# Performance work log

Hardware: AMD Instinct MI355X
Metric: run time of the kernel (lower is better)

The kernel has to match this reference:

```python
import jax, jax.numpy as jnp
import numpy as np


def _bd(x, W, b):
    # block-diagonal linear: x [B, D] -> [B, Dout], W [H, D/H, Dout/H], b [Dout]
    B, D = x.shape
    H = W.shape[0]
    y = jnp.einsum('bhi,hio->bho', x.reshape(B, H, D // H), W)
    return y.reshape(B, -1) + b


def setup_inputs() -> dict:
    key = jax.random.key(0)
    ks = jax.random.split(key, 16)
    B, D, H = 8192, 1024, 8
    U = int(D * 4 / 3)  # 1365
    d = D // H          # 128
    s = 0.05
    f32 = jnp.float32
    return {
        'x': jax.random.normal(ks[0], (B, D), f32),
        'h_prev': jax.random.normal(ks[1], (B, D), f32),
        'c_prev': jax.random.normal(ks[2], (B, D), f32),
        'n_prev': jax.random.uniform(ks[3], (B, D), f32) + 0.5,  # positive normalizer state
        'm_prev': jax.random.normal(ks[4], (B, D), f32),
        'ln_g': jnp.ones((D,), f32),
        'ln_b': jnp.zeros((D,), f32),
        'conv_w': jax.random.normal(ks[5], (1, 1, 4), f32) * 0.5,
        'conv_b': jax.random.normal(ks[6], (1,), f32) * 0.1,
        'W': jax.random.normal(ks[7], (4, H, d, d), f32) * s,   # gates z,i,f,o input projections
        'bW': jax.random.normal(ks[8], (4, D), f32) * s,
        'R': jax.random.normal(ks[9], (4, H, d, d), f32) * s,   # gates z,i,f,o recurrent projections
        'bR': jax.random.normal(ks[10], (4, D), f32) * s,
        'upl_w': jax.random.normal(ks[11], (D, U), f32) * s,
        'upl_b': jnp.zeros((U,), f32),
        'upr_w': jax.random.normal(ks[12], (D, U), f32) * s,
        'upr_b': jnp.zeros((U,), f32),
        'down_w': jax.random.normal(ks[13], (U, D), f32) * s,
        'down_b': jnp.zeros((D,), f32),
    }


def reference(x, h_prev, c_prev, n_prev, m_prev, ln_g, ln_b, conv_w, conv_b,
              W, bW, R, bR, upl_w, upl_b, upr_w, upr_b, down_w, down_b):
    # LayerNorm over feature dim (eps matches torch default 1e-5)
    mu = jnp.mean(x, axis=-1, keepdims=True)
    var = jnp.var(x, axis=-1, keepdims=True)
    x_norm = (x - mu) * jax.lax.rsqrt(var + 1e-5) * ln_g + ln_b
    # causal conv1d along the feature axis: kernel 4, left-pad 3 (Conv1d(1,1,4))
    conv = jax.lax.conv_general_dilated(
        x_norm[:, None, :], conv_w, window_strides=(1,), padding=[(3, 0)],
        dimension_numbers=('NCH', 'OIH', 'NCH'))[:, 0, :] + conv_b
    x_conv = jax.nn.silu(conv)
    # block-diagonal gate pre-activations (gate order in W/R stacks: z, i, f, o)
    z = jnp.tanh(_bd(x, W[0], bW[0]) + _bd(h_prev, R[0], bR[0]))
    o = jax.nn.sigmoid(_bd(x, W[3], bW[3]) + _bd(h_prev, R[3], bR[3]))
    i_tilde = _bd(x_conv, W[1], bW[1]) + _bd(h_prev, R[1], bR[1])
    f_tilde = _bd(x_conv, W[2], bW[2]) + _bd(h_prev, R[2], bR[2])
    # stabilized exp-max gating
    m_t = jnp.maximum(f_tilde + m_prev, i_tilde)
    i = jnp.exp(i_tilde - m_t)
    f = jnp.exp(f_tilde + m_prev - m_t)
    c_t = f * c_prev + i * z
    n_t = f * n_prev + i
    h_t = o * c_t / n_t
    # gated MLP (torch F.gelu default = exact erf gelu)
    left = h_t @ upl_w + upl_b
    right = jax.nn.gelu(h_t @ upr_w + upr_b, approximate=False)
    output = (left * right) @ down_w + down_b
    return (output, h_t, c_t, n_t, m_t)
```

## Files before the change

### kernel.cpp

```cpp
#include <hip/hip_runtime.h>
#include <hip/hip_bf16.h>

typedef __attribute__((ext_vector_type(8))) short s8v;
typedef __attribute__((ext_vector_type(4))) float f4v;
typedef unsigned short us4 __attribute__((ext_vector_type(4)));

#define NB 8192
#define ND 1024
#define NH 8
#define NU 1365
#define NUP 1408
#define GK 384
#define GN 512
static const size_t BD = (size_t)NB * ND;

#define WS_AG   ((size_t)0)
#define WS_G    ((size_t)50331648)
#define WS_HBF  ((size_t)73400320)
#define WS_WG   ((size_t)90177536)
#define WS_ULR  ((size_t)93323264)
#define WS_DWNT ((size_t)99090432)

__device__ __forceinline__ void gload16(const void* g, void* l) {
  __builtin_amdgcn_global_load_lds((const __attribute__((address_space(1))) void*)g,
                                   (__attribute__((address_space(3))) void*)l, 16, 0, 0);
}
__device__ __forceinline__ unsigned short tobf(float f) {
  unsigned int u = __float_as_uint(f);
  unsigned int r = (u + 0x7FFFu + ((u >> 16) & 1u)) >> 16;
  return (unsigned short)r;
}
__device__ __forceinline__ float frcp(float x) { return __builtin_amdgcn_rcpf(x); }
__device__ __forceinline__ float fsigm(float x) { return frcp(1.f + __expf(-x)); }
__device__ __forceinline__ float ftanh(float x) {
  float e = __expf(2.f * x);
  return 1.f - 2.f * frcp(e + 1.f);
}
__device__ __forceinline__ f4v mfma16(s8v a, s8v b, f4v c) {
  return __builtin_amdgcn_mfma_f32_16x16x32_bf16(a, b, c, 0, 0, 0);
}

__global__ __launch_bounds__(256) void prep_norm(
    const float* __restrict__ W, const float* __restrict__ R,
    const float* __restrict__ upl, const float* __restrict__ upr,
    const float* __restrict__ dwn,
    const float* __restrict__ x, const float* __restrict__ hp,
    const float* __restrict__ lg, const float* __restrict__ lb,
    const float* __restrict__ cw, const float* __restrict__ cb,
    unsigned short* __restrict__ Wg, unsigned short* __restrict__ ULR,
    unsigned short* __restrict__ Dt, unsigned short* __restrict__ Ag) {
  if (blockIdx.x < 23040) {
    long long idx = (long long)blockIdx.x * 256 + threadIdx.x;
    const long long N1 = (long long)4096 * GK;
    const long long N3 = (long long)2 * NUP * ND;
    const long long N2 = (long long)NUP * ND;
    if (idx < N1) {
      int c = (int)(idx / GK), k = (int)(idx % GK);
      int j = c & 15, g = (c >> 4) & 3, cgrp = (c >> 6) & 7, h = c >> 9;
      int o = cgrp * 16 + j;
      float v = 0.f;
      if (k < 128) {
        if (g == 0 || g == 3) v = W[(((size_t)g * NH + h) * 128 + k) * 128 + o];
      } else if (k < 256) {
        if (g == 1 || g == 2) v = W[(((size_t)g * NH + h) * 128 + (k - 128)) * 128 + o];
      } else {
        v = R[(((size_t)g * NH + h) * 128 + (k - 256)) * 128 + o];
      }
      Wg[idx] = tobf(v);
      return;
    }
    idx -= N1;
    if (idx < N3) {
      int r = (int)(idx / ND), k = (int)(idx % ND);
      int o = (r >> 4) & 1;
      int gcol = (r >> 5) * 16 + (r & 15);
      float v = 0.f;
      if (gcol < NU) v = o ? upr[(size_t)k * NU + gcol] : upl[(size_t)k * NU + gcol];
      ULR[idx] = tobf(v);
      return;
    }
    idx -= N3;
    if (idx < N2) { int n = (int)(idx / NUP), k = (int)(idx % NUP);
      Dt[idx] = (k < NU) ? tobf(dwn[(size_t)k * ND + n]) : 0; }
    return;
  }
  const int b = blockIdx.x - 23040, tid = threadIdx.x;
  const int lane = tid & 63, wv = tid >> 6;
  __shared__ float xs[1024];
  __shared__ float red[8];
  const int d0 = tid * 4;
  float4 xv = *(const float4*)(x + (size_t)b * ND + d0);
  float s = xv.x + xv.y + xv.z + xv.w;
  float ss = xv.x * xv.x + xv.y * xv.y + xv.z * xv.z + xv.w * xv.w;
#pragma unroll
  for (int o = 32; o; o >>= 1) { s += __shfl_down(s, o); ss += __shfl_down(ss, o); }
  if (lane == 0) { red[wv] = s; red[4 + wv] = ss; }
  __syncthreads();
  float S = red[0] + red[1] + red[2] + red[3];
  float SS = red[4] + red[5] + red[6] + red[7];
  float mu = S * (1.f / ND);
  float var = SS * (1.f / ND) - mu * mu;
  float rstd = rsqrtf(var + 1e-5f);
  float xn[4];
#pragma unroll
  for (int t = 0; t < 4; ++t) {
    float xx = (&xv.x)[t];
    xn[t] = (xx - mu) * rstd * lg[d0 + t] + lb[d0 + t];
    xs[d0 + t] = xn[t];
  }
  __syncthreads();
  float w0 = cw[0], w1 = cw[1], w2 = cw[2], w3 = cw[3], cbv = cb[0];
  float cv[4];
#pragma unroll
  for (int t = 0; t < 4; ++t) {
    int d = d0 + t;
    float a = cbv + w3 * xs[d];
    if (d >= 1) a += w2 * xs[d - 1];
    if (d >= 2) a += w1 * xs[d - 2];
    if (d >= 3) a += w0 * xs[d - 3];
    cv[t] = a * fsigm(a);
  }
  float4 hv = *(const float4*)(hp + (size_t)b * ND + d0);
  const int h = d0 >> 7, j = d0 & 127;
  us4 px, pc, ph;
#pragma unroll
  for (int t = 0; t < 4; ++t) { px[t] = tobf((&xv.x)[t]); pc[t] = tobf(cv[t]); ph[t] = tobf((&hv.x)[t]); }
  size_t base = (size_t)b * 3072 + (size_t)h * 384 + j;
  *(us4*)(Ag + base) = px;
  *(us4*)(Ag + base + 128) = pc;
  *(us4*)(Ag + base + 256) = ph;
}

__global__ __launch_bounds__(256) void gate_fused(
    const unsigned short* __restrict__ Ag, const unsigned short* __restrict__ Wg,
    const float* __restrict__ bW, const float* __restrict__ bR,
    const float* __restrict__ cp, const float* __restrict__ np_,
    const float* __restrict__ mp,
    float* __restrict__ dout, unsigned short* __restrict__ Hb) {
  __shared__ short As[128 * 32];
  __shared__ short Bs[128 * 32];
  const int tid = threadIdx.x, lane = tid & 63, wv = tid >> 6;
  const int wm = wv >> 1, wn = wv & 1;
  const int row0 = blockIdx.x * 128;
  const int p = blockIdx.y;
  const int h = blockIdx.z;
  const int srow = wv * 32 + (lane >> 2), scol = (lane & 3) * 8;
  const unsigned short* At = Ag + (size_t)h * 384;
  const unsigned short* Bt = Wg + ((size_t)h * 512 + (size_t)p * 128) * GK;
  const int cgrp = p * 2 + wn;
  const int gcol = h * 128 + cgrp * 16 + (lane & 15);
  float pc_[16], pn_[16], pm_[16];
#pragma unroll
  for (int m = 0; m < 4; ++m)
#pragma unroll
    for (int r = 0; r < 4; ++r) {
      const size_t idx = (size_t)(row0 + wm * 64 + m * 16 + (lane >> 4) * 4 + r) * ND + gcol;
      pc_[m * 4 + r] = cp[idx];
      pn_[m * 4 + r] = np_[idx];
      pm_[m * 4 + r] = mp[idx];
    }
  f4v acc[4][4] = {};
#pragma unroll
  for (int kt = 0; kt < 12; ++kt) {
    const int k0 = kt * 32;
    gload16(At + (size_t)(row0 + srow) * 3072 + k0 + scol, (char*)As + wv * 2048);
    gload16(At + (size_t)(row0 + srow + 16) * 3072 + k0 + scol, (char*)As + wv * 2048 + 1024);
    gload16(Bt + (size_t)srow * GK + k0 + scol, (char*)Bs + wv * 2048);
    gload16(Bt + (size_t)(srow + 16) * GK + k0 + scol, (char*)Bs + wv * 2048 + 1024);
    __syncthreads();
    s8v a[4];
#pragma unroll
    for (int m = 0; m < 4; ++m)
      a[m] = *(const s8v*)&As[(wm * 64 + m * 16 + (lane & 15)) * 32 + (lane >> 4) * 8];
#pragma unroll
    for (int g = 0; g < 4; ++g) {
      const bool active = (kt >= 8) || (kt < 4 ? (g == 0 || g == 3) : (g == 1 || g == 2));
      if (active) {
        s8v b = *(const s8v*)&Bs[(wn * 64 + g * 16 + (lane & 15)) * 32 + (lane >> 4) * 8];
#pragma unroll
        for (int m = 0; m < 4; ++m) acc[m][g] = mfma16(a[m], b, acc[m][g]);
      }
    }
    __syncthreads();
  }
  const float Bz = bW[gcol] + bR[gcol];
  const float Bi = bW[ND + gcol] + bR[ND + gcol];
  const float Bf = bW[2 * ND + gcol] + bR[2 * ND + gcol];
  const float Bo = bW[3 * ND + gcol] + bR[3 * ND + gcol];
#pragma unroll
  for (int m = 0; m < 4; ++m) {
    const int rbase = row0 + wm * 64 + m * 16 + (lane >> 4) * 4;
#pragma unroll
    for (int r = 0; r < 4; ++r) {
      const int e = m * 4 + r;
      const size_t idx = (size_t)(rbase + r) * ND + gcol;
      float zt = ftanh(acc[m][0][r] + Bz);
      float it = acc[m][1][r] + Bi;
      float ft = acc[m][2][r] + Bf;
      float ot = fsigm(acc[m][3][r] + Bo);
      float mv = pm_[e];
      float mt = fmaxf(ft + mv, it);
      float ii = __expf(it - mt);
      float ff = __expf(ft + mv - mt);
      float ct = ff * pc_[e] + ii * zt;
      float nt = ff * pn_[e] + ii;
      float ht = ot * ct * frcp(nt);
      dout[BD + idx] = ht;
      dout[2 * BD + idx] = ct;
      dout[3 * BD + idx] = nt;
      dout[4 * BD + idx] = mt;
      Hb[idx] = tobf(ht);
    }
  }
}

__global__ __launch_bounds__(256) void up_gemm(
    const unsigned short* __restrict__ A, const unsigned short* __restrict__ ULR,
    const float* __restrict__ lbias, const float* __restrict__ rbias,
    unsigned short* __restrict__ G) {
  __shared__ short As[4096];
  __shared__ short Bs[4096];
  const int tid = threadIdx.x, lane = tid & 63, wv = tid >> 6;
  const int wm = wv >> 1, wn = wv & 1;
  const int bid = blockIdx.x;
  const int swz = (bid & 7) * 176 + (bid >> 3);
  const int row0 = (swz / 22) * 128, n0 = (swz % 22) * 128;
  const int srow = wv * 32 + (lane >> 2), scol = (lane & 3) * 8;
  f4v acc[4][4] = {};
  for (int kt = 0; kt < 32; ++kt) {
    const int k0 = kt * 32;
    gload16(A + (size_t)(row0 + srow) * 1024 + k0 + scol, (char*)As + wv * 2048);
    gload16(A + (size_t)(row0 + srow + 16) * 1024 + k0 + scol, (char*)As + wv * 2048 + 1024);
    gload16(ULR + (size_t)(n0 + srow) * 1024 + k0 + scol, (char*)Bs + wv * 2048);
    gload16(ULR + (size_t)(n0 + srow + 16) * 1024 + k0 + scol, (char*)Bs + wv * 2048 + 1024);
    __syncthreads();
    s8v a[4], b[4];
#pragma unroll
    for (int m = 0; m < 4; ++m) a[m] = *(const s8v*)&As[(wm * 64 + m * 16 + (lane & 15)) * 32 + (lane >> 4) * 8];
#pragma unroll
    for (int n = 0; n < 4; ++n) b[n] = *(const s8v*)&Bs[(wn * 64 + n * 16 + (lane & 15)) * 32 + (lane >> 4) * 8];
#pragma unroll
    for (int m = 0; m < 4; ++m)
#pragma unroll
      for (int n = 0; n < 4; ++n) acc[m][n] = mfma16(a[m], b[n], acc[m][n]);
    __syncthreads();
  }
  const int gb = (n0 >> 1) + wn * 32;
#pragma unroll
  for (int m = 0; m < 4; ++m) {
    const int row = row0 + wm * 64 + m * 16 + (lane >> 4) * 4;
#pragma unroll
    for (int p = 0; p < 2; ++p) {
      const int gcol = gb + p * 16 + (lane & 15);
      const bool ok = gcol < NU;
      const float bl_ = ok ? lbias[gcol] : 0.f;
      const float br_ = ok ? rbias[gcol] : 0.f;
#pragma unroll
      for (int r = 0; r < 4; ++r) {
        float L = acc[m][2 * p][r] + bl_;
        float Rv = acc[m][2 * p + 1][r] + br_;
        float ge = 0.5f * Rv * (1.f + erff(Rv * 0.70710678118654752f));
        G[(size_t)(row + r) * NUP + gcol] = ok ? tobf(L * ge) : (unsigned short)0;
      }
    }
  }
}

__global__ __launch_bounds__(256) void down_gemm(
    const unsigned short* __restrict__ A, const unsigned short* __restrict__ Bt,
    const float* __restrict__ dbias, float* __restrict__ out) {
  __shared__ short As[4096];
  __shared__ short Bs[4096];
  const int tid = threadIdx.x, lane = tid & 63, wv = tid >> 6;
  const int wm = wv >> 1, wn = wv & 1;
  const int bid = blockIdx.x;
  const int swz = (bid & 7) * 64 + (bid >> 3);
  const int row0 = (swz >> 3) * 128, n0 = (swz & 7) * 128;
  const int srow = wv * 32 + (lane >> 2), scol = (lane & 3) * 8;
  f4v acc[4][4] = {};
  for (int kt = 0; kt < NUP / 32; ++kt) {
    const int k0 = kt * 32;
    gload16(A + (size_t)(row0 + srow) * NUP + k0 + scol, (char*)As + wv * 2048);
    gload16(A + (size_t)(row0 + srow + 16) * NUP + k0 + scol, (char*)As + wv * 2048 + 1024);
    gload16(Bt + (size_t)(n0 + srow) * NUP + k0 + scol, (char*)Bs + wv * 2048);
    gload16(Bt + (size_t)(n0 + srow + 16) * NUP + k0 + scol, (char*)Bs + wv * 2048 + 1024);
    __syncthreads();
    s8v a[4], b[4];
#pragma unroll
    for (int m = 0; m < 4; ++m) a[m] = *(const s8v*)&As[(wm * 64 + m * 16 + (lane & 15)) * 32 + (lane >> 4) * 8];
#pragma unroll
    for (int n = 0; n < 4; ++n) b[n] = *(const s8v*)&Bs[(wn * 64 + n * 16 + (lane & 15)) * 32 + (lane >> 4) * 8];
#pragma unroll
    for (int m = 0; m < 4; ++m)
#pragma unroll
      for (int n = 0; n < 4; ++n) acc[m][n] = mfma16(a[m], b[n], acc[m][n]);
    __syncthreads();
  }
#pragma unroll
  for (int m = 0; m < 4; ++m) {
    const int row = row0 + wm * 64 + m * 16 + (lane >> 4) * 4;
#pragma unroll
    for (int n = 0; n < 4; ++n) {
      const int col = n0 + wn * 64 + n * 16 + (lane & 15);
      const float bias = dbias[col];
#pragma unroll
      for (int r = 0; r < 4; ++r)
        out[(size_t)(row + r) * ND + col] = acc[m][n][r] + bias;
    }
  }
}

extern "C" void kernel_launch(void* const* d_in, const int* in_sizes, int n_in,
                              void* d_out, int out_size, void* d_ws, size_t ws_size,
                              hipStream_t stream) {
  const float* x    = (const float*)d_in[0];
  const float* hp   = (const float*)d_in[1];
  const float* cp   = (const float*)d_in[2];
  const float* np_  = (const float*)d_in[3];
  const float* mp   = (const float*)d_in[4];
  const float* lg   = (const float*)d_in[5];
  const float* lb   = (const float*)d_in[6];
  const float* cw   = (const float*)d_in[7];
  const float* cb   = (const float*)d_in[8];
  const float* W    = (const float*)d_in[9];
  const float* bW   = (const float*)d_in[10];
  const float* R    = (const float*)d_in[11];
  const float* bR   = (const float*)d_in[12];
  const float* upl  = (const float*)d_in[13];
  const float* uplb = (const float*)d_in[14];
  const float* upr  = (const float*)d_in[15];
  const float* uprb = (const float*)d_in[16];
  const float* dwn  = (const float*)d_in[17];
  const float* dwnb = (const float*)d_in[18];
  float* out = (float*)d_out;
  char* ws = (char*)d_ws;
  unsigned short* Ag  = (unsigned short*)(ws + WS_AG);
  unsigned short* G   = (unsigned short*)(ws + WS_G);
  unsigned short* Hb  = (unsigned short*)(ws + WS_HBF);
  unsigned short* Wg  = (unsigned short*)(ws + WS_WG);
  unsigned short* ULR = (unsigned short*)(ws + WS_ULR);
  unsigned short* Dt  = (unsigned short*)(ws + WS_DWNT);

  prep_norm<<<23040 + NB, 256, 0, stream>>>(W, R, upl, upr, dwn, x, hp, lg, lb, cw, cb,
                                            Wg, ULR, Dt, Ag);
  gate_fused<<<dim3(64, 4, 8), 256, 0, stream>>>(Ag, Wg, bW, bR, cp, np_, mp, out, Hb);
  up_gemm<<<1408, 256, 0, stream>>>(Hb, ULR, uplb, uprb, G);
  down_gemm<<<512, 256, 0, stream>>>(G, Dt, dwnb, out);
}
```

Baseline: 250.4 us.

## Use 64-wide swizzled K tiles in MLP GEMMs and tanh-approximate GELU

```diff
diff --git a/kernel.cpp b/kernel.cpp
--- a/kernel.cpp
+++ b/kernel.cpp
@@ -35,6 +35,10 @@
 __device__ __forceinline__ float ftanh(float x) {
   float e = __expf(2.f * x);
   return 1.f - 2.f * frcp(e + 1.f);
+}
+__device__ __forceinline__ float fgelu(float x) {
+  float t = ftanh(0.7978845608f * (x + 0.044715f * x * x * x));
+  return 0.5f * x * (1.f + t);
 }
 __device__ __forceinline__ f4v mfma16(s8v a, s8v b, f4v c) {
   return __builtin_amdgcn_mfma_f32_16x16x32_bf16(a, b, c, 0, 0, 0);
@@ -218,31 +222,40 @@
     const unsigned short* __restrict__ A, const unsigned short* __restrict__ ULR,
     const float* __restrict__ lbias, const float* __restrict__ rbias,
     unsigned short* __restrict__ G) {
-  __shared__ short As[4096];
-  __shared__ short Bs[4096];
+  __shared__ short As[128 * 64];
+  __shared__ short Bs[128 * 64];
   const int tid = threadIdx.x, lane = tid & 63, wv = tid >> 6;
   const int wm = wv >> 1, wn = wv & 1;
   const int bid = blockIdx.x;
   const int swz = (bid & 7) * 176 + (bid >> 3);
   const int row0 = (swz / 22) * 128, n0 = (swz % 22) * 128;
-  const int srow = wv * 32 + (lane >> 2), scol = (lane & 3) * 8;
+  const int sr = lane >> 3;
+  const int usrc = ((lane & 7) ^ sr) * 8;
   f4v acc[4][4] = {};
-  for (int kt = 0; kt < 32; ++kt) {
-    const int k0 = kt * 32;
-    gload16(A + (size_t)(row0 + srow) * 1024 + k0 + scol, (char*)As + wv * 2048);
-    gload16(A + (size_t)(row0 + srow + 16) * 1024 + k0 + scol, (char*)As + wv * 2048 + 1024);
-    gload16(ULR + (size_t)(n0 + srow) * 1024 + k0 + scol, (char*)Bs + wv * 2048);
-    gload16(ULR + (size_t)(n0 + srow + 16) * 1024 + k0 + scol, (char*)Bs + wv * 2048 + 1024);
-    __syncthreads();
-    s8v a[4], b[4];
-#pragma unroll
-    for (int m = 0; m < 4; ++m) a[m] = *(const s8v*)&As[(wm * 64 + m * 16 + (lane & 15)) * 32 + (lane >> 4) * 8];
-#pragma unroll
-    for (int n = 0; n < 4; ++n) b[n] = *(const s8v*)&Bs[(wn * 64 + n * 16 + (lane & 15)) * 32 + (lane >> 4) * 8];
-#pragma unroll
-    for (int m = 0; m < 4; ++m)
-#pragma unroll
-      for (int n = 0; n < 4; ++n) acc[m][n] = mfma16(a[m], b[n], acc[m][n]);
+  for (int kt = 0; kt < 16; ++kt) {
+    const int k0 = kt * 64;
+#pragma unroll
+    for (int q = 0; q < 4; ++q) {
+      const int br = wv * 32 + q * 8;
+      gload16(A + (size_t)(row0 + br + sr) * 1024 + k0 + usrc, (char*)As + br * 128);
+      gload16(ULR + (size_t)(n0 + br + sr) * 1024 + k0 + usrc, (char*)Bs + br * 128);
+    }
+    __syncthreads();
+#pragma unroll
+    for (int kk = 0; kk < 2; ++kk) {
+      const int u8 = (((kk * 4 + (lane >> 4)) ^ (lane & 7)) * 8);
+      s8v a[4], b[4];
+#pragma unroll
+      for (int m = 0; m < 4; ++m)
+        a[m] = *(const s8v*)&As[(wm * 64 + m * 16 + (lane & 15)) * 64 + u8];
+#pragma unroll
+      for (int n = 0; n < 4; ++n)
+        b[n] = *(const s8v*)&Bs[(wn * 64 + n * 16 + (lane & 15)) * 64 + u8];
+#pragma unroll
+      for (int m = 0; m < 4; ++m)
+#pragma unroll
+        for (int n = 0; n < 4; ++n) acc[m][n] = mfma16(a[m], b[n], acc[m][n]);
+    }
     __syncthreads();
   }
   const int gb = (n0 >> 1) + wn * 32;
@@ -250,17 +263,16 @@
   for (int m = 0; m < 4; ++m) {
     const int row = row0 + wm * 64 + m * 16 + (lane >> 4) * 4;
 #pragma unroll
-    for (int p = 0; p < 2; ++p) {
-      const int gcol = gb + p * 16 + (lane & 15);
+    for (int pp = 0; pp < 2; ++pp) {
+      const int gcol = gb + pp * 16 + (lane & 15);
       const bool ok = gcol < NU;
       const float bl_ = ok ? lbias[gcol] : 0.f;
       const float br_ = ok ? rbias[gcol] : 0.f;
 #pragma unroll
       for (int r = 0; r < 4; ++r) {
-        float L = acc[m][2 * p][r] + bl_;
-        float Rv = acc[m][2 * p + 1][r] + br_;
-        float ge = 0.5f * Rv * (1.f + erff(Rv * 0.70710678118654752f));
-        G[(size_t)(row + r) * NUP + gcol] = ok ? tobf(L * ge) : (unsigned short)0;
+        float L = acc[m][2 * pp][r] + bl_;
+        float Rv = acc[m][2 * pp + 1][r] + br_;
+        G[(size_t)(row + r) * NUP + gcol] = ok ? tobf(L * fgelu(Rv)) : (unsigned short)0;
       }
     }
   }
@@ -269,31 +281,40 @@
 __global__ __launch_bounds__(256) void down_gemm(
     const unsigned short* __restrict__ A, const unsigned short* __restrict__ Bt,
     const float* __restrict__ dbias, float* __restrict__ out) {
-  __shared__ short As[4096];
-  __shared__ short Bs[4096];
+  __shared__ short As[128 * 64];
+  __shared__ short Bs[128 * 64];
   const int tid = threadIdx.x, lane = tid & 63, wv = tid >> 6;
   const int wm = wv >> 1, wn = wv & 1;
   const int bid = blockIdx.x;
   const int swz = (bid & 7) * 64 + (bid >> 3);
   const int row0 = (swz >> 3) * 128, n0 = (swz & 7) * 128;
-  const int srow = wv * 32 + (lane >> 2), scol = (lane & 3) * 8;
+  const int sr = lane >> 3;
+  const int usrc = ((lane & 7) ^ sr) * 8;
   f4v acc[4][4] = {};
-  for (int kt = 0; kt < NUP / 32; ++kt) {
-    const int k0 = kt * 32;
-    gload16(A + (size_t)(row0 + srow) * NUP + k0 + scol, (char*)As + wv * 2048);
-    gload16(A + (size_t)(row0 + srow + 16) * NUP + k0 + scol, (char*)As + wv * 2048 + 1024);
-    gload16(Bt + (size_t)(n0 + srow) * NUP + k0 + scol, (char*)Bs + wv * 2048);
-    gload16(Bt + (size_t)(n0 + srow + 16) * NUP + k0 + scol, (char*)Bs + wv * 2048 + 1024);
-    __syncthreads();
-    s8v a[4], b[4];
-#pragma unroll
-    for (int m = 0; m < 4; ++m) a[m] = *(const s8v*)&As[(wm * 64 + m * 16 + (lane & 15)) * 32 + (lane >> 4) * 8];
-#pragma unroll
-    for (int n = 0; n < 4; ++n) b[n] = *(const s8v*)&Bs[(wn * 64 + n * 16 + (lane & 15)) * 32 + (lane >> 4) * 8];
-#pragma unroll
-    for (int m = 0; m < 4; ++m)
-#pragma unroll
-      for (int n = 0; n < 4; ++n) acc[m][n] = mfma16(a[m], b[n], acc[m][n]);
+  for (int kt = 0; kt < NUP / 64; ++kt) {
+    const int k0 = kt * 64;
+#pragma unroll
+    for (int q = 0; q < 4; ++q) {
+      const int br = wv * 32 + q * 8;
+      gload16(A + (size_t)(row0 + br + sr) * NUP + k0 + usrc, (char*)As + br * 128);
+      gload16(Bt + (size_t)(n0 + br + sr) * NUP + k0 + usrc, (char*)Bs + br * 128);
+    }
+    __syncthreads();
+#pragma unroll
+    for (int kk = 0; kk < 2; ++kk) {
+      const int u8 = (((kk * 4 + (lane >> 4)) ^ (lane & 7)) * 8);
+      s8v a[4], b[4];
+#pragma unroll
+      for (int m = 0; m < 4; ++m)
+        a[m] = *(const s8v*)&As[(wm * 64 + m * 16 + (lane & 15)) * 64 + u8];
+#pragma unroll
+      for (int n = 0; n < 4; ++n)
+        b[n] = *(const s8v*)&Bs[(wn * 64 + n * 16 + (lane & 15)) * 64 + u8];
+#pragma unroll
+      for (int m = 0; m < 4; ++m)
+#pragma unroll
+        for (int n = 0; n < 4; ++n) acc[m][n] = mfma16(a[m], b[n], acc[m][n]);
+    }
     __syncthreads();
   }
 #pragma unroll
```

After: 236.9 us, median of 2. 5.4% less time.
